# Kernel optimization log

Hardware: AMD Instinct MI355X
Metric: run time of the kernel (lower is better)

## Reference

```python
import jax, jax.numpy as jnp
import numpy as np


def setup_inputs() -> dict:
    key = jax.random.key(0)
    k1, k2, k3, k4 = jax.random.split(key, 4)
    N, E, C_in, C_out = 50000, 625000, 256, 128
    x = jax.random.normal(k1, (N, C_in), dtype=jnp.float32)
    W = jax.random.normal(k2, (C_out, C_in), dtype=jnp.float32) * (1.0 / np.sqrt(C_in))
    b = jax.random.normal(k3, (C_out,), dtype=jnp.float32) * 0.01
    edge_index = jax.random.randint(k4, (2, E), 0, N, dtype=jnp.int64)
    return {"x": x, "W": W, "b": b, "edge_index": edge_index}


def reference(x, W, b, edge_index):
    # x: [N, C_in], W: [C_out, C_in], b: [C_out], edge_index: [2, E]
    N = x.shape[0]
    h = jnp.dot(x, W.T) + b  # [N, C_out] (nn.Linear)
    r, c = edge_index[0], edge_index[1]
    # node degree via scatter_add of ones over destination index r
    deg = jax.ops.segment_sum(jnp.ones(r.shape[0], dtype=h.dtype), r, num_segments=N)
    # rsqrt with inf (deg==0) replaced by 0
    nd_rsqrt = jnp.where(deg > 0, jax.lax.rsqrt(jnp.maximum(deg, 1.0)), jnp.zeros_like(deg))
    # gather messages from source nodes c, normalize by source rsqrt-degree
    message_norm = h[c] * nd_rsqrt[c][:, None]  # [E, C_out]
    # scatter-add to destination nodes r
    out = jax.ops.segment_sum(message_norm, r, num_segments=N)  # [N, C_out]
    # final destination-side normalization
    return out * nd_rsqrt[:, None]
```

## Files before the change

kernel.cpp:

```cpp
#include <hip/hip_runtime.h>

#define C_IN 256
#define C_OUT 128
#define ELL_PAD 64
#define BUCK_CAP 4096
#define EDGES_PER_BLK 4096

typedef __attribute__((ext_vector_type(8))) short bf16x8;
typedef __attribute__((ext_vector_type(8))) unsigned short ushort8;
typedef __attribute__((ext_vector_type(4))) float f32x4;

__device__ inline unsigned short f2bf(float f) {
    unsigned u = __builtin_bit_cast(unsigned, f);
    unsigned r = (u + 0x7FFFu + ((u >> 16) & 1u)) >> 16;
    return (unsigned short)r;
}
__device__ inline float bflo(unsigned u) { return __builtin_bit_cast(float, u << 16); }
__device__ inline float bfhi(unsigned u) { return __builtin_bit_cast(float, u & 0xFFFF0000u); }

__global__ __launch_bounds__(256) void wconv_zero_kernel(const float* __restrict__ W,
                                                         unsigned short* __restrict__ WB,
                                                         int* __restrict__ bucket_cnt, int nbuck) {
    int ci = blockIdx.x * 256 + threadIdx.x;
    int q = ci & 3, cl = (ci >> 2) & 15, ctt = ci >> 6;
    int colw = (ctt & 7) * 16 + cl;
    int k0 = (ctt >> 3) * 32 + q * 8;
    const float* src = W + colw * C_IN + k0;
    bf16x8 o;
    #pragma unroll
    for (int j = 0; j < 8; ++j) o[j] = (short)f2bf(src[j]);
    *(bf16x8*)(WB + (size_t)ci * 8) = o;
    if (ci < nbuck) bucket_cnt[ci] = 0;
}

__global__ __launch_bounds__(256) void bucketize_kernel(const int* __restrict__ ridx,
                                                        const int* __restrict__ cidx,
                                                        int* __restrict__ bucket_cnt,
                                                        unsigned* __restrict__ buckets,
                                                        int E, int nbuck) {
    __shared__ unsigned stage[EDGES_PER_BLK];
    __shared__ int cnt[256];
    __shared__ int base[256];
    __shared__ int off[256];
    int t = threadIdx.x;
    int e0 = blockIdx.x * EDGES_PER_BLK;
    int nv = E - e0; if (nv > EDGES_PER_BLK) nv = EDGES_PER_BLK;

    cnt[t] = 0;
    __syncthreads();

    for (int k = t; k < nv; k += 256) {
        int r = ridx[e0 + k];
        int c = cidx[e0 + k];
        stage[k] = ((unsigned)r << 16) | (unsigned)c;
        atomicAdd(&cnt[r >> 8], 1);
    }
    __syncthreads();

    if (t < nbuck) {
        int cb = cnt[t];
        base[t] = (cb > 0) ? atomicAdd(&bucket_cnt[t], cb) : 0;
    }
    off[t] = 0;
    __syncthreads();

    for (int k = t; k < nv; k += 256) {
        unsigned v = stage[k];
        int bkt = (int)(v >> 24);
        int p = atomicAdd(&off[bkt], 1);
        int dst = base[bkt] + p;
        if (dst < BUCK_CAP)
            buckets[(size_t)bkt * BUCK_CAP + dst] = v;
    }
}

__global__ __launch_bounds__(256) void build_ell_kernel(const int* __restrict__ bucket_cnt,
                                                        const unsigned* __restrict__ buckets,
                                                        int* __restrict__ deg,
                                                        unsigned short* __restrict__ col_ell, int N) {
    __shared__ int cur[256];
    __shared__ unsigned short ell[256 * ELL_PAD];
    int t = threadIdx.x;
    int b = blockIdx.x;
    cur[t] = 0;
    __syncthreads();

    int cnt = bucket_cnt[b];
    if (cnt > BUCK_CAP) cnt = BUCK_CAP;
    const unsigned* bb = buckets + (size_t)b * BUCK_CAP;
    for (int e = t; e < cnt; e += 256) {
        unsigned v = bb[e];
        int rl = (v >> 16) & 255;
        int pos = atomicAdd(&cur[rl], 1);
        if (pos < ELL_PAD)
            ell[rl * ELL_PAD + pos] = (unsigned short)(v & 0xFFFFu);
    }
    __syncthreads();

    int node = (b << 8) + t;
    if (node < N) {
        int d = cur[t];
        deg[node] = d;
        if (d > ELL_PAD) d = ELL_PAD;
        int chunks = (d + 7) >> 3;
        ushort8* dst = (ushort8*)(col_ell + (size_t)node * ELL_PAD);
        const ushort8* src = (const ushort8*)(ell + t * ELL_PAD);
        for (int j = 0; j < chunks; ++j) dst[j] = src[j];
    }
}

__global__ __launch_bounds__(256) void gemm_kernel(const float* __restrict__ x,
                                                   const unsigned short* __restrict__ WB,
                                                   const float* __restrict__ b,
                                                   unsigned short* __restrict__ h, int N) {
    int tid = threadIdx.x;
    int w = tid >> 6, l = tid & 63;
    int row0 = blockIdx.x * 64;
    int lq = l >> 4, lr = l & 15;

    int arow = row0 + w * 16 + lr;
    bool rowok = (arow < N);
    const float* xr = x + (size_t)(rowok ? arow : 0) * C_IN + lq * 8;
    const char* wb = (const char*)WB;
    int boff = lr * 64 + lq * 16;

    f32x4 acc[8];
    #pragma unroll
    for (int ct = 0; ct < 8; ++ct) acc[ct] = (f32x4){0.f, 0.f, 0.f, 0.f};

    #pragma unroll
    for (int t = 0; t < 8; ++t) {
        float4 v0 = make_float4(0.f, 0.f, 0.f, 0.f);
        float4 v1 = make_float4(0.f, 0.f, 0.f, 0.f);
        if (rowok) {
            v0 = *(const float4*)(xr + t * 32);
            v1 = *(const float4*)(xr + t * 32 + 4);
        }
        bf16x8 af;
        af[0] = (short)f2bf(v0.x); af[1] = (short)f2bf(v0.y);
        af[2] = (short)f2bf(v0.z); af[3] = (short)f2bf(v0.w);
        af[4] = (short)f2bf(v1.x); af[5] = (short)f2bf(v1.y);
        af[6] = (short)f2bf(v1.z); af[7] = (short)f2bf(v1.w);
        #pragma unroll
        for (int ct = 0; ct < 8; ++ct) {
            bf16x8 bfv = *(const bf16x8*)(wb + (t * 8 + ct) * 1024 + boff);
            acc[ct] = __builtin_amdgcn_mfma_f32_16x16x32_bf16(af, bfv, acc[ct], 0, 0, 0);
        }
    }

    #pragma unroll
    for (int ct = 0; ct < 8; ++ct) {
        int colc = ct * 16 + lr;
        float bv = b[colc];
        #pragma unroll
        for (int r = 0; r < 4; ++r) {
            int grow = row0 + w * 16 + lq * 4 + r;
            if (grow < N)
                h[(size_t)grow * C_OUT + colc] = f2bf(acc[ct][r] + bv);
        }
    }
}

__global__ __launch_bounds__(256) void gather_kernel(const int* __restrict__ deg,
                                                     const unsigned short* __restrict__ col_ell,
                                                     const unsigned short* __restrict__ h,
                                                     float* __restrict__ out, int N) {
    int gid = blockIdx.x * 256 + threadIdx.x;
    int node = gid >> 6;
    if (node >= N) return;
    int lane = threadIdx.x & 63;
    int nb = lane >> 4, lr = lane & 15;

    int d = deg[node];
    float sv = (d > 0) ? rsqrtf((float)d) : 0.0f;
    int dd = (d > ELL_PAD) ? ELL_PAD : d;
    const unsigned short* cl = col_ell + (size_t)node * ELL_PAD;
    const char* hb = (const char*)h;

    float acc[8] = {0.f, 0.f, 0.f, 0.f, 0.f, 0.f, 0.f, 0.f};
    for (int i = nb; i < dd; i += 4) {
        int c = cl[i];
        uint4 v = *(const uint4*)(hb + (size_t)c * (C_OUT * 2) + lr * 16);
        int dc = deg[c];
        float sc = (dc > 0) ? rsqrtf((float)dc) : 0.0f;
        acc[0] += sc * bflo(v.x); acc[1] += sc * bfhi(v.x);
        acc[2] += sc * bflo(v.y); acc[3] += sc * bfhi(v.y);
        acc[4] += sc * bflo(v.z); acc[5] += sc * bfhi(v.z);
        acc[6] += sc * bflo(v.w); acc[7] += sc * bfhi(v.w);
    }
    #pragma unroll
    for (int j = 0; j < 8; ++j) {
        acc[j] += __shfl_xor(acc[j], 16, 64);
        acc[j] += __shfl_xor(acc[j], 32, 64);
    }
    if (nb == 0) {
        float4 o0 = make_float4(acc[0] * sv, acc[1] * sv, acc[2] * sv, acc[3] * sv);
        float4 o1 = make_float4(acc[4] * sv, acc[5] * sv, acc[6] * sv, acc[7] * sv);
        float* op = out + (size_t)node * C_OUT + lr * 8;
        *(float4*)(op)     = o0;
        *(float4*)(op + 4) = o1;
    }
}

extern "C" void kernel_launch(void* const* d_in, const int* in_sizes, int n_in,
                              void* d_out, int out_size, void* d_ws, size_t ws_size,
                              hipStream_t stream) {
    const float* x = (const float*)d_in[0];
    const float* W = (const float*)d_in[1];
    const float* b = (const float*)d_in[2];
    const int*   ei = (const int*)d_in[3];
    float* out = (float*)d_out;

    int N = in_sizes[0] / C_IN;
    int E = in_sizes[3] / 2;
    const int* ridx = ei;
    const int* cidx = ei + E;

    int nbuck = (N + 255) >> 8;

    char* wsc = (char*)d_ws;
    unsigned short* h  = (unsigned short*)wsc;       wsc += (size_t)N * C_OUT * sizeof(unsigned short);
    unsigned short* WB = (unsigned short*)wsc;       wsc += (size_t)C_OUT * C_IN * sizeof(unsigned short);
    int*   deg      = (int*)wsc;                     wsc += (size_t)N * sizeof(int);
    unsigned short* col_ell = (unsigned short*)wsc;  wsc += (size_t)N * ELL_PAD * sizeof(unsigned short);
    int*   bucket_cnt = (int*)wsc;                   wsc += (size_t)nbuck * sizeof(int);
    unsigned* buckets = (unsigned*)wsc;

    wconv_zero_kernel<<<16, 256, 0, stream>>>(W, WB, bucket_cnt, nbuck);

    bucketize_kernel<<<(E + EDGES_PER_BLK - 1) / EDGES_PER_BLK, 256, 0, stream>>>(
        ridx, cidx, bucket_cnt, buckets, E, nbuck);

    build_ell_kernel<<<nbuck, 256, 0, stream>>>(bucket_cnt, buckets, deg, col_ell, N);

    gemm_kernel<<<(N + 63) / 64, 256, 0, stream>>>(x, WB, b, h, N);

    long long gth = (long long)N * 64;
    gather_kernel<<<(int)((gth + 255) / 256), 256, 0, stream>>>(deg, col_ell, h, out, N);
}
```

Before: 86.64 us.

## Merge bucketize and GEMM into one interleaved launch; precompute rsqrt degrees

The edge-bucketize blocks and the GEMM blocks now run in a single grid, with bucket blocks spread evenly among GEMM blocks, so the latency-bound bucketing overlaps with the compute-bound projection and one launch is saved. The build_ell kernel also writes a per-node rsqrt-degree array, so the gather reads one float per neighbor instead of loading the degree and computing rsqrt for every edge. This adds an extra N-float workspace array and a heavier shared-memory footprint for the GEMM blocks, since they share a kernel with the bucketizer's LDS staging, which can reduce occupancy.

```diff
diff --git a/kernel.cpp b/kernel.cpp
--- a/kernel.cpp
+++ b/kernel.cpp
@@ -33,50 +33,111 @@
     if (ci < nbuck) bucket_cnt[ci] = 0;
 }
 
-__global__ __launch_bounds__(256) void bucketize_kernel(const int* __restrict__ ridx,
-                                                        const int* __restrict__ cidx,
-                                                        int* __restrict__ bucket_cnt,
-                                                        unsigned* __restrict__ buckets,
-                                                        int E, int nbuck) {
+__global__ __launch_bounds__(256) void fused_bucket_gemm(const float* __restrict__ x,
+                                                         const unsigned short* __restrict__ WB,
+                                                         const float* __restrict__ b,
+                                                         const int* __restrict__ ridx,
+                                                         const int* __restrict__ cidx,
+                                                         int* __restrict__ bucket_cnt,
+                                                         unsigned* __restrict__ buckets,
+                                                         unsigned short* __restrict__ h,
+                                                         int N, int E, int nbuck, int G_bkt) {
     __shared__ unsigned stage[EDGES_PER_BLK];
     __shared__ int cnt[256];
     __shared__ int base[256];
     __shared__ int off[256];
     int t = threadIdx.x;
-    int e0 = blockIdx.x * EDGES_PER_BLK;
-    int nv = E - e0; if (nv > EDGES_PER_BLK) nv = EDGES_PER_BLK;
-
-    cnt[t] = 0;
-    __syncthreads();
-
-    for (int k = t; k < nv; k += 256) {
-        int r = ridx[e0 + k];
-        int c = cidx[e0 + k];
-        stage[k] = ((unsigned)r << 16) | (unsigned)c;
-        atomicAdd(&cnt[r >> 8], 1);
-    }
-    __syncthreads();
-
-    if (t < nbuck) {
-        int cb = cnt[t];
-        base[t] = (cb > 0) ? atomicAdd(&bucket_cnt[t], cb) : 0;
-    }
-    off[t] = 0;
-    __syncthreads();
-
-    for (int k = t; k < nv; k += 256) {
-        unsigned v = stage[k];
-        int bkt = (int)(v >> 24);
-        int p = atomicAdd(&off[bkt], 1);
-        int dst = base[bkt] + p;
-        if (dst < BUCK_CAP)
-            buckets[(size_t)bkt * BUCK_CAP + dst] = v;
+
+    int T = gridDim.x;
+    long long i = blockIdx.x;
+    int f_i  = (int)((i * (long long)G_bkt) / T);
+    int f_i1 = (int)(((i + 1) * (long long)G_bkt) / T);
+
+    if (f_i1 > f_i) {
+        int e0 = f_i * EDGES_PER_BLK;
+        int nv = E - e0; if (nv > EDGES_PER_BLK) nv = EDGES_PER_BLK;
+
+        cnt[t] = 0;
+        __syncthreads();
+
+        for (int k = t; k < nv; k += 256) {
+            int r = ridx[e0 + k];
+            int c = cidx[e0 + k];
+            stage[k] = ((unsigned)r << 16) | (unsigned)c;
+            atomicAdd(&cnt[r >> 8], 1);
+        }
+        __syncthreads();
+
+        if (t < nbuck) {
+            int cb = cnt[t];
+            base[t] = (cb > 0) ? atomicAdd(&bucket_cnt[t], cb) : 0;
+        }
+        off[t] = 0;
+        __syncthreads();
+
+        for (int k = t; k < nv; k += 256) {
+            unsigned v = stage[k];
+            int bkt = (int)(v >> 24);
+            int p = atomicAdd(&off[bkt], 1);
+            int dst = base[bkt] + p;
+            if (dst < BUCK_CAP)
+                buckets[(size_t)bkt * BUCK_CAP + dst] = v;
+        }
+        return;
+    }
+
+    int gemmId = (int)i - f_i;
+    int w = t >> 6, l = t & 63;
+    int row0 = gemmId * 64;
+    int lq = l >> 4, lr = l & 15;
+
+    int arow = row0 + w * 16 + lr;
+    bool rowok = (arow < N);
+    const float* xr = x + (size_t)(rowok ? arow : 0) * C_IN + lq * 8;
+    const char* wb = (const char*)WB;
+    int boff = lr * 64 + lq * 16;
+
+    f32x4 acc[8];
+    #pragma unroll
+    for (int ct = 0; ct < 8; ++ct) acc[ct] = (f32x4){0.f, 0.f, 0.f, 0.f};
+
+    #pragma unroll
+    for (int tt = 0; tt < 8; ++tt) {
+        float4 v0 = make_float4(0.f, 0.f, 0.f, 0.f);
+        float4 v1 = make_float4(0.f, 0.f, 0.f, 0.f);
+        if (rowok) {
+            v0 = *(const float4*)(xr + tt * 32);
+            v1 = *(const float4*)(xr + tt * 32 + 4);
+        }
+        bf16x8 af;
+        af[0] = (short)f2bf(v0.x); af[1] = (short)f2bf(v0.y);
+        af[2] = (short)f2bf(v0.z); af[3] = (short)f2bf(v0.w);
+        af[4] = (short)f2bf(v1.x); af[5] = (short)f2bf(v1.y);
+        af[6] = (short)f2bf(v1.z); af[7] = (short)f2bf(v1.w);
+        #pragma unroll
+        for (int ct = 0; ct < 8; ++ct) {
+            bf16x8 bfv = *(const bf16x8*)(wb + (tt * 8 + ct) * 1024 + boff);
+            acc[ct] = __builtin_amdgcn_mfma_f32_16x16x32_bf16(af, bfv, acc[ct], 0, 0, 0);
+        }
+    }
+
+    #pragma unroll
+    for (int ct = 0; ct < 8; ++ct) {
+        int colc = ct * 16 + lr;
+        float bv = b[colc];
+        #pragma unroll
+        for (int r = 0; r < 4; ++r) {
+            int grow = row0 + w * 16 + lq * 4 + r;
+            if (grow < N)
+                h[(size_t)grow * C_OUT + colc] = f2bf(acc[ct][r] + bv);
+        }
     }
 }
 
 __global__ __launch_bounds__(256) void build_ell_kernel(const int* __restrict__ bucket_cnt,
                                                         const unsigned* __restrict__ buckets,
                                                         int* __restrict__ deg,
+                                                        float* __restrict__ s,
                                                         unsigned short* __restrict__ col_ell, int N) {
     __shared__ int cur[256];
     __shared__ unsigned short ell[256 * ELL_PAD];
@@ -101,6 +162,7 @@
     if (node < N) {
         int d = cur[t];
         deg[node] = d;
+        s[node] = (d > 0) ? rsqrtf((float)d) : 0.0f;
         if (d > ELL_PAD) d = ELL_PAD;
         int chunks = (d + 7) >> 3;
         ushort8* dst = (ushort8*)(col_ell + (size_t)node * ELL_PAD);
@@ -109,59 +171,8 @@
     }
 }
 
-__global__ __launch_bounds__(256) void gemm_kernel(const float* __restrict__ x,
-                                                   const unsigned short* __restrict__ WB,
-                                                   const float* __restrict__ b,
-                                                   unsigned short* __restrict__ h, int N) {
-    int tid = threadIdx.x;
-    int w = tid >> 6, l = tid & 63;
-    int row0 = blockIdx.x * 64;
-    int lq = l >> 4, lr = l & 15;
-
-    int arow = row0 + w * 16 + lr;
-    bool rowok = (arow < N);
-    const float* xr = x + (size_t)(rowok ? arow : 0) * C_IN + lq * 8;
-    const char* wb = (const char*)WB;
-    int boff = lr * 64 + lq * 16;
-
-    f32x4 acc[8];
-    #pragma unroll
-    for (int ct = 0; ct < 8; ++ct) acc[ct] = (f32x4){0.f, 0.f, 0.f, 0.f};
-
-    #pragma unroll
-    for (int t = 0; t < 8; ++t) {
-        float4 v0 = make_float4(0.f, 0.f, 0.f, 0.f);
-        float4 v1 = make_float4(0.f, 0.f, 0.f, 0.f);
-        if (rowok) {
-            v0 = *(const float4*)(xr + t * 32);
-            v1 = *(const float4*)(xr + t * 32 + 4);
-        }
-        bf16x8 af;
-        af[0] = (short)f2bf(v0.x); af[1] = (short)f2bf(v0.y);
-        af[2] = (short)f2bf(v0.z); af[3] = (short)f2bf(v0.w);
-        af[4] = (short)f2bf(v1.x); af[5] = (short)f2bf(v1.y);
-        af[6] = (short)f2bf(v1.z); af[7] = (short)f2bf(v1.w);
-        #pragma unroll
-        for (int ct = 0; ct < 8; ++ct) {
-            bf16x8 bfv = *(const bf16x8*)(wb + (t * 8 + ct) * 1024 + boff);
-            acc[ct] = __builtin_amdgcn_mfma_f32_16x16x32_bf16(af, bfv, acc[ct], 0, 0, 0);
-        }
-    }
-
-    #pragma unroll
-    for (int ct = 0; ct < 8; ++ct) {
-        int colc = ct * 16 + lr;
-        float bv = b[colc];
-        #pragma unroll
-        for (int r = 0; r < 4; ++r) {
-            int grow = row0 + w * 16 + lq * 4 + r;
-            if (grow < N)
-                h[(size_t)grow * C_OUT + colc] = f2bf(acc[ct][r] + bv);
-        }
-    }
-}
-
 __global__ __launch_bounds__(256) void gather_kernel(const int* __restrict__ deg,
+                                                     const float* __restrict__ s,
                                                      const unsigned short* __restrict__ col_ell,
                                                      const unsigned short* __restrict__ h,
                                                      float* __restrict__ out, int N) {
@@ -172,7 +183,7 @@
     int nb = lane >> 4, lr = lane & 15;
 
     int d = deg[node];
-    float sv = (d > 0) ? rsqrtf((float)d) : 0.0f;
+    float sv = s[node];
     int dd = (d > ELL_PAD) ? ELL_PAD : d;
     const unsigned short* cl = col_ell + (size_t)node * ELL_PAD;
     const char* hb = (const char*)h;
@@ -181,8 +192,7 @@
     for (int i = nb; i < dd; i += 4) {
         int c = cl[i];
         uint4 v = *(const uint4*)(hb + (size_t)c * (C_OUT * 2) + lr * 16);
-        int dc = deg[c];
-        float sc = (dc > 0) ? rsqrtf((float)dc) : 0.0f;
+        float sc = s[c];
         acc[0] += sc * bflo(v.x); acc[1] += sc * bfhi(v.x);
         acc[2] += sc * bflo(v.y); acc[3] += sc * bfhi(v.y);
         acc[4] += sc * bflo(v.z); acc[5] += sc * bfhi(v.z);
@@ -222,19 +232,21 @@
     unsigned short* h  = (unsigned short*)wsc;       wsc += (size_t)N * C_OUT * sizeof(unsigned short);
     unsigned short* WB = (unsigned short*)wsc;       wsc += (size_t)C_OUT * C_IN * sizeof(unsigned short);
     int*   deg      = (int*)wsc;                     wsc += (size_t)N * sizeof(int);
+    float* s        = (float*)wsc;                   wsc += (size_t)N * sizeof(float);
     unsigned short* col_ell = (unsigned short*)wsc;  wsc += (size_t)N * ELL_PAD * sizeof(unsigned short);
     int*   bucket_cnt = (int*)wsc;                   wsc += (size_t)nbuck * sizeof(int);
     unsigned* buckets = (unsigned*)wsc;
 
     wconv_zero_kernel<<<16, 256, 0, stream>>>(W, WB, bucket_cnt, nbuck);
 
-    bucketize_kernel<<<(E + EDGES_PER_BLK - 1) / EDGES_PER_BLK, 256, 0, stream>>>(
-        ridx, cidx, bucket_cnt, buckets, E, nbuck);
-
-    build_ell_kernel<<<nbuck, 256, 0, stream>>>(bucket_cnt, buckets, deg, col_ell, N);
-
-    gemm_kernel<<<(N + 63) / 64, 256, 0, stream>>>(x, WB, b, h, N);
+    int G_bkt  = (E + EDGES_PER_BLK - 1) / EDGES_PER_BLK;
+    int G_gemm = (N + 63) / 64;
+    fused_bucket_gemm<<<G_bkt + G_gemm, 256, 0, stream>>>(x, WB, b, ridx, cidx,
+                                                          bucket_cnt, buckets, h,
+                                                          N, E, nbuck, G_bkt);
+
+    build_ell_kernel<<<nbuck, 256, 0, stream>>>(bucket_cnt, buckets, deg, s, col_ell, N);
 
     long long gth = (long long)N * 64;
-    gather_kernel<<<(int)((gth + 255) / 256), 256, 0, stream>>>(deg, col_ell, h, out, N);
-}
+    gather_kernel<<<(int)((gth + 255) / 256), 256, 0, stream>>>(deg, s, col_ell, h, out, N);
+}
```

Result: faster. 75.50 us (-12.9%).
